# Kernel optimization log

Hardware: AMD Instinct MI355X
Metric: run time of the kernel (lower is better)

Reference implementation:

```python
import jax, jax.numpy as jnp
import numpy as np

B, T, ZDIM, H = 16384, 60, 6, 100
ATEMP = 5.0


def setup_inputs() -> dict:
    key = jax.random.key(0)
    ks = jax.random.split(key, 12)
    sampled_z = jax.random.normal(ks[0], (B, ZDIM), jnp.float32)
    u = jax.random.uniform(ks[1], (B, 5), jnp.float32)
    # physically plausible, strictly positive IDM params:
    # desired_v ~ [20,30], tgap ~ [1,2], min_jamx ~ [1,4], max/min act ~ [1,3]
    idm_params = jnp.stack([20. + 10. * u[:, 0], 1. + u[:, 1], 1. + 3. * u[:, 2],
                            1. + 2. * u[:, 3], 1. + 2. * u[:, 4]], axis=-1)
    # idm_s cols: [ego_v, f_v, m_v, ego_x, f_x, m_x, ef_dv, ef_dx, em_dv, em_dx, f_exists, m_exists]
    vels = jax.random.uniform(ks[2], (B, T, 3), jnp.float32, 0., 30.)
    glx = jax.random.uniform(ks[3], (B, T, 3), jnp.float32, 0., 500.)
    dvs = jax.random.normal(ks[4], (B, T, 2), jnp.float32) * 2.0
    dxs = jax.random.uniform(ks[5], (B, T, 2), jnp.float32, 5., 100.)
    ex = (jax.random.uniform(ks[6], (B, T, 2)) > 0.2).astype(jnp.float32)
    idm_s = jnp.concatenate([vels[:, :, 0:1], vels[:, :, 1:2], vels[:, :, 2:3],
                             glx[:, :, 0:1], glx[:, :, 1:2], glx[:, :, 2:3],
                             dvs[:, :, 0:1], dxs[:, :, 0:1],
                             dvs[:, :, 1:2], dxs[:, :, 1:2], ex], axis=-1)
    sdv_acts = jax.random.normal(ks[7], (B, T, 1), jnp.float32) * 0.5
    W1 = jax.random.normal(ks[8], (ZDIM, H), jnp.float32) * 0.1
    b1 = jnp.zeros((H,), jnp.float32)
    Wi = jax.random.normal(ks[9], (H + 1, 4 * H), jnp.float32) * 0.1
    Wh = jax.random.normal(ks[10], (H, 4 * H), jnp.float32) * 0.1
    bl = jnp.zeros((4 * H,), jnp.float32)
    Wa = jax.random.normal(ks[11], (H, 1), jnp.float32) * 0.1
    ba = jnp.zeros((1,), jnp.float32)
    return dict(sampled_z=sampled_z, idm_params=idm_params, idm_s=idm_s, sdv_acts=sdv_acts,
                W1=W1, b1=b1, Wi=Wi, Wh=Wh, bl=bl, Wa=Wa, ba=ba)


def _idm_driver(vel, dv, dx, p):
    dx = jnp.clip(dx, 0.5, 1000.0)
    desired_v, tgap, jamx = p[:, 0:1], p[:, 1:2], p[:, 2:3]
    amax, amin = p[:, 3:4], p[:, 4:5]
    gap = jamx + jax.nn.relu(tgap * vel + vel * dv / (2.0 * jnp.sqrt(amax * amin)))
    act = amax * (1.0 - (vel / desired_v) ** 4 - (gap / dx) ** 2)
    return jnp.clip(act, -3.0, 3.0)  # action_clip


def reference(sampled_z, idm_params, idm_s, sdv_acts, W1, b1, Wi, Wh, bl, Wa, ba):
    Bn = sampled_z.shape[0]
    proj = sampled_z @ W1 + b1                       # [B,100] latent projection
    nkey = jax.random.key(42)
    noise_f = jax.random.normal(jax.random.fold_in(nkey, 0), (T, Bn, 1), proj.dtype) * 0.5
    noise_m = jax.random.normal(jax.random.fold_in(nkey, 1), (T, Bn, 1), proj.dtype) * 0.5
    s_seq = jnp.transpose(idm_s, (1, 0, 2))          # [T,B,12]
    a_seq = jnp.transpose(sdv_acts, (1, 0, 2))       # [T,B,1]

    def step(carry, xs):
        ego_v, ego_x, prev_act, h, c = carry
        s, sdv, nf, nm, t = xs
        is0 = (t == 0)
        ego_v = jnp.where(is0, s[:, 0:1], ego_v + prev_act * 0.1)
        ego_x = jnp.where(is0, s[:, 3:4], ego_x + ego_v * 0.1 + 0.5 * prev_act * 0.01)
        fex, mex = s[:, 10:11], s[:, 11:12]
        ef_dx = (s[:, 4:5] - ego_x) * fex + (1.0 - fex) * s[:, 7:8]
        em_dx = (s[:, 5:6] - ego_x) * mex + (1.0 - mex) * s[:, 9:10]
        ef_dv = (ego_v - s[:, 1:2]) * fex + (1.0 - fex) * s[:, 6:7]
        em_dv = (ego_v - s[:, 2:3]) * mex + (1.0 - mex) * s[:, 8:9]
        ef_act = _idm_driver(ego_v, ef_dv, ef_dx, idm_params)
        ef_act = fex * ef_act + (1.0 - fex) * nf      # add_noise for nonexisting cars
        em_act = _idm_driver(ego_v, em_dv, em_dx, idm_params)
        em_act = mex * em_act + (1.0 - mex) * nm
        x = jnp.concatenate([proj, sdv], axis=-1)     # [B,101]
        z = x @ Wi + h @ Wh + bl                      # [B,400], keras gate order i,f,g,o
        i, f, g, o = jnp.split(z, 4, axis=-1)
        c = jax.nn.sigmoid(f) * c + jax.nn.sigmoid(i) * jnp.tanh(g)
        h = jax.nn.sigmoid(o) * jnp.tanh(c)
        att = jax.nn.sigmoid(ATEMP * (h @ Wa + ba))   # 1/(1+exp(-temp*x))
        act = (1.0 - att) * ef_act + att * em_act
        return (ego_v, ego_x, act, h, c), (act, att)

    z0 = jnp.zeros((Bn, 1), proj.dtype)
    carry0 = (z0, z0, z0, proj, proj)
    _, (acts, atts) = jax.lax.scan(step, carry0, (s_seq, a_seq, noise_f, noise_m, jnp.arange(T)))
    return jnp.transpose(acts, (1, 0, 2)), jnp.transpose(atts, (1, 0, 2))
```

## Files before the change

### kernel.cpp

```cpp
#include <hip/hip_runtime.h>
#include <cstdint>
#include <cstddef>

#define BTOT   16384
#define TSTEPS 60
#define HDIM   100
#define GDIM   400
#define NB     64
#define NTHR   1024

static_assert(BTOT % NB == 0, "batch tiling");

typedef __attribute__((ext_vector_type(8))) short bf16x8;
typedef __attribute__((ext_vector_type(4))) float f32x4;
typedef __attribute__((ext_vector_type(4))) unsigned int u32x4;

struct TFPair { uint32_t a, b; };

__host__ __device__ constexpr uint32_t rotl32c(uint32_t v, int r){
  return (v << r) | (v >> (32 - r));
}

__host__ __device__ constexpr TFPair tf2x32(uint32_t k0, uint32_t k1,
                                            uint32_t x0, uint32_t x1){
  const uint32_t ks2 = k0 ^ k1 ^ 0x1BD11BDAu;
  x0 += k0; x1 += k1;
  x0 += x1; x1 = rotl32c(x1,13); x1 ^= x0;
  x0 += x1; x1 = rotl32c(x1,15); x1 ^= x0;
  x0 += x1; x1 = rotl32c(x1,26); x1 ^= x0;
  x0 += x1; x1 = rotl32c(x1, 6); x1 ^= x0;
  x0 += k1;  x1 += ks2 + 1u;
  x0 += x1; x1 = rotl32c(x1,17); x1 ^= x0;
  x0 += x1; x1 = rotl32c(x1,29); x1 ^= x0;
  x0 += x1; x1 = rotl32c(x1,16); x1 ^= x0;
  x0 += x1; x1 = rotl32c(x1,24); x1 ^= x0;
  x0 += ks2; x1 += k0 + 2u;
  x0 += x1; x1 = rotl32c(x1,13); x1 ^= x0;
  x0 += x1; x1 = rotl32c(x1,15); x1 ^= x0;
  x0 += x1; x1 = rotl32c(x1,26); x1 ^= x0;
  x0 += x1; x1 = rotl32c(x1, 6); x1 ^= x0;
  x0 += k0;  x1 += k1 + 3u;
  x0 += x1; x1 = rotl32c(x1,17); x1 ^= x0;
  x0 += x1; x1 = rotl32c(x1,29); x1 ^= x0;
  x0 += x1; x1 = rotl32c(x1,16); x1 ^= x0;
  x0 += x1; x1 = rotl32c(x1,24); x1 ^= x0;
  x0 += k1;  x1 += ks2 + 4u;
  x0 += x1; x1 = rotl32c(x1,13); x1 ^= x0;
  x0 += x1; x1 = rotl32c(x1,15); x1 ^= x0;
  x0 += x1; x1 = rotl32c(x1,26); x1 ^= x0;
  x0 += x1; x1 = rotl32c(x1, 6); x1 ^= x0;
  x0 += ks2; x1 += k0 + 5u;
  return TFPair{x0, x1};
}

constexpr TFPair KF = tf2x32(0u, 42u, 0u, 0u);
constexpr TFPair KM = tf2x32(0u, 42u, 0u, 1u);

__device__ __forceinline__ float rcp_fast(float x){ return __builtin_amdgcn_rcpf(x); }
__device__ __forceinline__ float sigmoid_f(float x){ return rcp_fast(1.f + __expf(-x)); }
__device__ __forceinline__ float tanh_f(float x){
  float e = __expf(2.f * x);
  return 1.f - 2.f * rcp_fast(e + 1.f);
}

__device__ __forceinline__ float tf_noise(uint32_t k0, uint32_t k1, uint32_t n){
  TFPair r = tf2x32(k0, k1, 0u, n);
  uint32_t bits = r.a ^ r.b;
  float u = __uint_as_float((bits >> 9) | 0x3f800000u) - 1.0f;
  const float LOV = -0.99999994f;
  float v = fmaxf(LOV, fmaf(u, 2.0f, LOV));
  float w = -log1pf(-v * v);
  float p;
  if (w < 5.0f){
    w -= 2.5f;
    p =              2.81022636e-08f;
    p = fmaf(p, w,   3.43273939e-07f);
    p = fmaf(p, w,  -3.5233877e-06f);
    p = fmaf(p, w,  -4.39150654e-06f);
    p = fmaf(p, w,   0.00021858087f);
    p = fmaf(p, w,  -0.00125372503f);
    p = fmaf(p, w,  -0.00417768164f);
    p = fmaf(p, w,   0.246640727f);
    p = fmaf(p, w,   1.50140941f);
  } else {
    w = sqrtf(w) - 3.0f;
    p =             -0.000200214257f;
    p = fmaf(p, w,   0.000100950558f);
    p = fmaf(p, w,   0.00134934322f);
    p = fmaf(p, w,  -0.00367342844f);
    p = fmaf(p, w,   0.00573950773f);
    p = fmaf(p, w,  -0.0076224613f);
    p = fmaf(p, w,   0.00943887047f);
    p = fmaf(p, w,   1.00167406f);
    p = fmaf(p, w,   2.83297682f);
  }
  return 0.70710678f * (p * v);
}

__device__ __forceinline__ float idm_act(float vel, float dv, float dx,
                                         float v0, float tg, float jx,
                                         float am, float an){
  dx = fminf(fmaxf(dx, 0.5f), 1000.0f);
  float gap = jx + fmaxf(0.0f, tg*vel + vel*dv / (2.0f * sqrtf(am*an)));
  float r  = vel / v0;  float r2 = r*r;
  float gd = gap / dx;
  float a  = am * (1.0f - r2*r2 - gd*gd);
  return fminf(fmaxf(a, -3.0f), 3.0f);
}

__device__ __forceinline__ unsigned short f2bf(float f){
  uint32_t x = __float_as_uint(f);
  return (unsigned short)((x + 0x7fffu + ((x >> 16) & 1u)) >> 16);
}
__device__ __forceinline__ float bf2f(unsigned short h){
  return __uint_as_float(((uint32_t)h) << 16);
}

#define FRG_PACKETS (25*4*64)
#define WS_WI_HI 51200
#define WS_WI_LO 102400
#define WHF_HW   51200

__global__ void build_frags_kernel(const float* __restrict__ Wi,
                                   const float* __restrict__ Wh,
                                   unsigned short* __restrict__ ws){
  int p = blockIdx.x * 256 + threadIdx.x;
  if (p >= FRG_PACKETS) return;
  int lane = p & 63;
  int kf   = (p >> 6) & 3;
  int mt   = p >> 8;
  int zc   = mt*16 + (lane & 15);
  int orig = (zc & 3)*100 + (zc >> 2);
  int kb   = kf*32 + ((lane >> 4) << 3);
  #pragma unroll
  for (int j = 0; j < 8; ++j){
    int k = kb + j;
    float vh = (k < HDIM) ? Wh[(size_t)k*GDIM + orig] : 0.f;
    float vi = (k < HDIM) ? Wi[(size_t)k*GDIM + orig] : 0.f;
    unsigned short ih = f2bf(vi);
    ws[p*8 + j]            = f2bf(vh);
    ws[WS_WI_HI + p*8 + j] = ih;
    ws[WS_WI_LO + p*8 + j] = f2bf(vi - bf2f(ih));
  }
}

#define HBF_HW (2*4*4*512)
__device__ __forceinline__ int hfr_idx(int hl, int bt, int kf, int lp, int j){
  return (((hl*4 + bt)*4 + kf)*512 + lp*8 + j);
}

__device__ __forceinline__ void mfma1(f32x4 (&acc)[4][2],
                                      const unsigned short* __restrict__ whf,
                                      const unsigned short* __restrict__ hbf,
                                      int nmt, int mt0, int bt0, int lane){
  #pragma unroll
  for (int kf = 0; kf < 4; ++kf){
    bf16x8 Bh0 = *(const bf16x8*)&hbf[hfr_idx(0, bt0+0, kf, lane, 0)];
    bf16x8 Bh1 = *(const bf16x8*)&hbf[hfr_idx(0, bt0+1, kf, lane, 0)];
    #pragma unroll
    for (int m = 0; m < 4; ++m){
      if (m < nmt){
        bf16x8 Ah = *(const bf16x8*)&whf[((mt0 + m)*4 + kf)*512 + lane*8];
        acc[m][0] = __builtin_amdgcn_mfma_f32_16x16x32_bf16(Ah, Bh0, acc[m][0], 0,0,0);
        acc[m][1] = __builtin_amdgcn_mfma_f32_16x16x32_bf16(Ah, Bh1, acc[m][1], 0,0,0);
      }
    }
  }
}

__device__ __forceinline__ void mfma3_wi(f32x4 (&acc)[4][2],
                                         const unsigned short* __restrict__ frg,
                                         const unsigned short* __restrict__ hbf,
                                         int nmt, int mt0, int bt0, int lane){
  #pragma unroll
  for (int kf = 0; kf < 4; ++kf){
    bf16x8 Bh0 = *(const bf16x8*)&hbf[hfr_idx(0, bt0+0, kf, lane, 0)];
    bf16x8 Bl0 = *(const bf16x8*)&hbf[hfr_idx(1, bt0+0, kf, lane, 0)];
    bf16x8 Bh1 = *(const bf16x8*)&hbf[hfr_idx(0, bt0+1, kf, lane, 0)];
    bf16x8 Bl1 = *(const bf16x8*)&hbf[hfr_idx(1, bt0+1, kf, lane, 0)];
    #pragma unroll
    for (int m = 0; m < 4; ++m){
      if (m < nmt){
        int pidx = ((mt0 + m)*4 + kf)*64 + lane;
        bf16x8 Ah = *(const bf16x8*)(frg + WS_WI_HI + (size_t)pidx*8);
        bf16x8 Al = *(const bf16x8*)(frg + WS_WI_LO + (size_t)pidx*8);
        acc[m][0] = __builtin_amdgcn_mfma_f32_16x16x32_bf16(Ah, Bh0, acc[m][0], 0,0,0);
        acc[m][0] = __builtin_amdgcn_mfma_f32_16x16x32_bf16(Ah, Bl0, acc[m][0], 0,0,0);
        acc[m][0] = __builtin_amdgcn_mfma_f32_16x16x32_bf16(Al, Bh0, acc[m][0], 0,0,0);
        acc[m][1] = __builtin_amdgcn_mfma_f32_16x16x32_bf16(Ah, Bh1, acc[m][1], 0,0,0);
        acc[m][1] = __builtin_amdgcn_mfma_f32_16x16x32_bf16(Ah, Bl1, acc[m][1], 0,0,0);
        acc[m][1] = __builtin_amdgcn_mfma_f32_16x16x32_bf16(Al, Bh1, acc[m][1], 0,0,0);
      }
    }
  }
}

__global__ __attribute__((amdgpu_flat_work_group_size(NTHR, NTHR),
                          amdgpu_waves_per_eu(4, 4)))
void idm_sim_kernel(const float* __restrict__ sampled_z,
                    const float* __restrict__ idm_params,
                    const float* __restrict__ idm_s,
                    const float* __restrict__ sdv_acts,
                    const float* __restrict__ W1,
                    const float* __restrict__ b1,
                    const float* __restrict__ Wi,
                    const float* __restrict__ bl,
                    const float* __restrict__ Wa,
                    const float* __restrict__ ba,
                    const unsigned short* __restrict__ frg,
                    float* __restrict__ out)
{
  __shared__ __align__(16) unsigned short whf[WHF_HW];
  __shared__ __align__(16) unsigned short hbf[HBF_HW];
  __shared__ float part_lds[32*64];
  __shared__ float noise_lds[2][2][NB];
  __shared__ float blp_lds[GDIM];
  __shared__ float wi100p_lds[GDIM];

  const int tid  = threadIdx.x;
  const int lane = tid & 63;
  const int wid  = __builtin_amdgcn_readfirstlane(tid >> 6);
  const int b0   = blockIdx.x * NB;
  const int bg   = b0 + lane;

  const int bt0 = (wid >> 3) * 2;
  const int w8  = wid & 7;
  const int nmt = (w8 == 0) ? 1 : ((w8 == 7) ? 0 : 4);
  const int mt0 = (w8 == 0) ? 0 : 1 + (w8 - 1)*4;
  const int lg  = lane >> 4;
  const int li  = lane & 15;

  for (int i = tid; i < WHF_HW/8; i += NTHR)
    ((u32x4*)whf)[i] = ((const u32x4*)frg)[i];
  for (int i = tid; i < HBF_HW/8; i += NTHR)
    ((u32x4*)hbf)[i] = (u32x4)(0u);
  for (int i = tid; i < GDIM; i += NTHR){
    int g = i & 3, c = i >> 2;
    blp_lds[i]    = bl[g*100 + c];
    wi100p_lds[i] = Wi[(size_t)HDIM*GDIM + g*100 + c];
  }
  __syncthreads();

  for (int idx = tid; idx < HDIM*NB; idx += NTHR){
    int k = idx >> 6;
    int b = idx & 63;
    const float* szp = sampled_z + (size_t)(b0 + b) * 6;
    float v = b1[k];
    #pragma unroll
    for (int z = 0; z < 6; ++z) v = fmaf(szp[z], W1[z*HDIM + k], v);
    unsigned short hi = f2bf(v);
    unsigned short lo = f2bf(v - bf2f(hi));
    int bt = b >> 4;
    int kf = k >> 5, lp = (b & 15) + (((k & 31) >> 3) << 4), j = k & 7;
    hbf[hfr_idx(0, bt, kf, lp, j)] = hi;
    hbf[hfr_idx(1, bt, kf, lp, j)] = lo;
  }

  float wa_reg[4];
  float c_reg[4][2];
  #pragma unroll
  for (int m = 0; m < 4; ++m){
    if (m < nmt){
      int c = (mt0 + m)*4 + lg;
      wa_reg[m] = Wa[c];
      #pragma unroll
      for (int b2 = 0; b2 < 2; ++b2){
        int b = b0 + (bt0 + b2)*16 + li;
        const float* szp = sampled_z + (size_t)b * 6;
        float v = b1[c];
        #pragma unroll
        for (int z = 0; z < 6; ++z) v = fmaf(szp[z], W1[z*HDIM + c], v);
        c_reg[m][b2] = v;
      }
    }
  }
  __syncthreads();

  float xzs[4][2][4];
  if (nmt > 0){
    f32x4 acc[4][2];
    #pragma unroll
    for (int m = 0; m < 4; ++m){
      if (m < nmt){
        int zb = (mt0 + m)*16 + lg*4;
        f32x4 blv = *(const f32x4*)&blp_lds[zb];
        acc[m][0] = blv; acc[m][1] = blv;
      }
    }
    mfma3_wi(acc, frg, hbf, nmt, mt0, bt0, lane);
    #pragma unroll
    for (int m = 0; m < 4; ++m) if (m < nmt)
      #pragma unroll
      for (int b2 = 0; b2 < 2; ++b2)
        #pragma unroll
        for (int r = 0; r < 4; ++r) xzs[m][b2][r] = acc[m][b2][r];
  }

  float p_v0=0.f, p_tg=0.f, p_jx=0.f, p_am=0.f, p_an=0.f;
  if (wid == 0){
    const float* pp = idm_params + (size_t)bg * 5;
    p_v0 = pp[0]; p_tg = pp[1]; p_jx = pp[2]; p_am = pp[3]; p_an = pp[4];
  }
  float ego_v = 0.f, ego_x = 0.f, prev_act = 0.f;
  const float ba0 = ba[0];
  const int bb0 = b0 + bt0*16 + li;

  for (int t = 0; t < TSTEPS; ++t){
    float efa = 0.f, ema = 0.f, fex = 0.f, mex = 0.f;
    if (wid == 0){
      const float* sp = idm_s + ((size_t)bg * TSTEPS + t) * 12;
      float4 s0 = *(const float4*)(sp);
      float4 s1 = *(const float4*)(sp + 4);
      float4 s2 = *(const float4*)(sp + 8);
      if (t == 0){ ego_v = s0.x; ego_x = s0.w; }
      else {
        ego_v = ego_v + prev_act * 0.1f;
        ego_x = ego_x + ego_v * 0.1f + 0.5f * prev_act * 0.01f;
      }
      fex = s2.z; mex = s2.w;
      float ef_dx = (s1.x - ego_x)*fex + (1.f-fex)*s1.w;
      float em_dx = (s1.y - ego_x)*mex + (1.f-mex)*s2.y;
      float ef_dv = (ego_v - s0.y)*fex + (1.f-fex)*s1.z;
      float em_dv = (ego_v - s0.z)*mex + (1.f-mex)*s2.x;
      efa = idm_act(ego_v, ef_dv, ef_dx, p_v0, p_tg, p_jx, p_am, p_an);
      ema = idm_act(ego_v, em_dv, em_dx, p_v0, p_tg, p_jx, p_am, p_an);
    } else if (wid == 7){
      noise_lds[t & 1][0][lane] = tf_noise(KF.a, KF.b, (uint32_t)(t*BTOT + bg));
    } else if (wid == 15){
      noise_lds[t & 1][1][lane] = tf_noise(KM.a, KM.b, (uint32_t)(t*BTOT + bg));
    }

    f32x4 acc[4][2];
    if (nmt > 0){
      float sdv0 = sdv_acts[(size_t)bb0 * TSTEPS + t];
      float sdv1 = sdv_acts[(size_t)(bb0 + 16) * TSTEPS + t];
      #pragma unroll
      for (int m = 0; m < 4; ++m){
        if (m < nmt){
          int zb = (mt0 + m)*16 + lg*4;
          f32x4 wiv = *(const f32x4*)&wi100p_lds[zb];
          #pragma unroll
          for (int r = 0; r < 4; ++r){
            acc[m][0][r] = fmaf(sdv0, wiv[r], xzs[m][0][r]);
            acc[m][1][r] = fmaf(sdv1, wiv[r], xzs[m][1][r]);
          }
        }
      }
      mfma1(acc, whf, hbf, nmt, mt0, bt0, lane);
    }
    __syncthreads();

    float part0 = 0.f, part1 = 0.f;
    #pragma unroll
    for (int m = 0; m < 4; ++m){
      if (m < nmt){
        int c  = (mt0 + m)*4 + lg;
        int kf = c >> 5, lp = li + (((c & 31) >> 3) << 4), j = c & 7;
        #pragma unroll
        for (int b2 = 0; b2 < 2; ++b2){
          float zi = acc[m][b2][0];
          float zf = acc[m][b2][1];
          float zg = acc[m][b2][2];
          float zo = acc[m][b2][3];
          float cn = fmaf(sigmoid_f(zf), c_reg[m][b2], sigmoid_f(zi) * tanh_f(zg));
          c_reg[m][b2] = cn;
          float h = sigmoid_f(zo) * tanh_f(cn);
          hbf[hfr_idx(0, bt0 + b2, kf, lp, j)] = f2bf(h);
          float pw = h * wa_reg[m];
          if (b2 == 0) part0 += pw; else part1 += pw;
        }
      }
    }
    part_lds[(wid*2 + 0)*64 + lane] = part0;
    part_lds[(wid*2 + 1)*64 + lane] = part1;
    __syncthreads();

    if (wid == 0){
      int half = lane >> 5;
      int b2g  = (lane >> 4) & 1;
      int bi   = lane & 15;
      float dot = ba0;
      #pragma unroll
      for (int w = 0; w < 8; ++w)
        #pragma unroll
        for (int res = 0; res < 4; ++res)
          dot += part_lds[((half*8 + w)*2 + b2g)*64 + res*16 + bi];
      float att = sigmoid_f(5.0f * dot);
      float nf = noise_lds[t & 1][0][lane];
      float nm = noise_lds[t & 1][1][lane];
      float efb = fex*efa + (1.f-fex)*nf;
      float emb = mex*ema + (1.f-mex)*nm;
      float act = (1.f - att) * efb + att * emb;
      prev_act = act;
      out[(size_t)bg * TSTEPS + t] = act;
      out[(size_t)BTOT*TSTEPS + (size_t)bg * TSTEPS + t] = att;
    }
  }
}

extern "C" void kernel_launch(void* const* d_in, const int* in_sizes, int n_in,
                              void* d_out, int out_size, void* d_ws, size_t ws_size,
                              hipStream_t stream) {
  (void)in_sizes; (void)n_in; (void)ws_size; (void)out_size;
  const float* sampled_z  = (const float*)d_in[0];
  const float* idm_params = (const float*)d_in[1];
  const float* idm_s      = (const float*)d_in[2];
  const float* sdv_acts   = (const float*)d_in[3];
  const float* W1         = (const float*)d_in[4];
  const float* b1         = (const float*)d_in[5];
  const float* Wi         = (const float*)d_in[6];
  const float* Wh         = (const float*)d_in[7];
  const float* bl         = (const float*)d_in[8];
  const float* Wa         = (const float*)d_in[9];
  const float* ba         = (const float*)d_in[10];
  float* out = (float*)d_out;
  unsigned short* frg = (unsigned short*)d_ws;

  build_frags_kernel<<<25, 256, 0, stream>>>(Wi, Wh, frg);
  dim3 grid(BTOT / NB);
  dim3 block(NTHR);
  idm_sim_kernel<<<grid, block, 0, stream>>>(sampled_z, idm_params, idm_s, sdv_acts,
                                             W1, b1, Wi, bl, Wa, ba, frg, out);
}
```

Baseline: 338.2 us.

## Double-buffer LSTM hidden state and partials to drop one barrier per step

The hidden-state fragment buffer and the attention partial-sum buffer are double-buffered by step parity, which removes the barrier that used to sit between the MFMA read of h and the write of the new h. The idm_s and sdv_acts loads for the next step are issued one iteration early and carried in registers to hide global latency. The cost is extra LDS for a second copy of the h and partial buffers, plus extra live registers. Correctness depends on the single remaining barrier per step ordering the parity-indexed buffers correctly, and HBF_HW already reserves two halves.

After: 440.8 us. 1.3x slower.

```diff
diff --git a/kernel.cpp b/kernel.cpp
--- a/kernel.cpp
+++ b/kernel.cpp
@@ -152,11 +152,11 @@
 __device__ __forceinline__ void mfma1(f32x4 (&acc)[4][2],
                                       const unsigned short* __restrict__ whf,
                                       const unsigned short* __restrict__ hbf,
-                                      int nmt, int mt0, int bt0, int lane){
+                                      int cur, int nmt, int mt0, int bt0, int lane){
   #pragma unroll
   for (int kf = 0; kf < 4; ++kf){
-    bf16x8 Bh0 = *(const bf16x8*)&hbf[hfr_idx(0, bt0+0, kf, lane, 0)];
-    bf16x8 Bh1 = *(const bf16x8*)&hbf[hfr_idx(0, bt0+1, kf, lane, 0)];
+    bf16x8 Bh0 = *(const bf16x8*)&hbf[hfr_idx(cur, bt0+0, kf, lane, 0)];
+    bf16x8 Bh1 = *(const bf16x8*)&hbf[hfr_idx(cur, bt0+1, kf, lane, 0)];
     #pragma unroll
     for (int m = 0; m < 4; ++m){
       if (m < nmt){
@@ -212,7 +212,7 @@
 {
   __shared__ __align__(16) unsigned short whf[WHF_HW];
   __shared__ __align__(16) unsigned short hbf[HBF_HW];
-  __shared__ float part_lds[32*64];
+  __shared__ float part_lds[2][32*64];
   __shared__ float noise_lds[2][2][NB];
   __shared__ float blp_lds[GDIM];
   __shared__ float wi100p_lds[GDIM];
@@ -295,6 +295,7 @@
         #pragma unroll
         for (int r = 0; r < 4; ++r) xzs[m][b2][r] = acc[m][b2][r];
   }
+  __syncthreads();
 
   float p_v0=0.f, p_tg=0.f, p_jx=0.f, p_am=0.f, p_an=0.f;
   if (wid == 0){
@@ -305,35 +306,60 @@
   const float ba0 = ba[0];
   const int bb0 = b0 + bt0*16 + li;
 
+  float4 cs0 = {}, cs1 = {}, cs2 = {};
+  float csdv0 = 0.f, csdv1 = 0.f;
+  if (wid == 0){
+    const float* sp = idm_s + ((size_t)bg * TSTEPS + 0) * 12;
+    cs0 = *(const float4*)(sp);
+    cs1 = *(const float4*)(sp + 4);
+    cs2 = *(const float4*)(sp + 8);
+  }
+  if (nmt > 0){
+    csdv0 = sdv_acts[(size_t)bb0 * TSTEPS + 0];
+    csdv1 = sdv_acts[(size_t)(bb0 + 16) * TSTEPS + 0];
+  }
+
+  int cur = 0;
   for (int t = 0; t < TSTEPS; ++t){
+    const int nxt = cur ^ 1;
+    const int par = t & 1;
+    const int tp  = (t + 1 < TSTEPS) ? t + 1 : t;
+
+    float4 ns0, ns1, ns2;
+    float nsdv0, nsdv1;
+    if (wid == 0){
+      const float* sp = idm_s + ((size_t)bg * TSTEPS + tp) * 12;
+      ns0 = *(const float4*)(sp);
+      ns1 = *(const float4*)(sp + 4);
+      ns2 = *(const float4*)(sp + 8);
+    }
+    if (nmt > 0){
+      nsdv0 = sdv_acts[(size_t)bb0 * TSTEPS + tp];
+      nsdv1 = sdv_acts[(size_t)(bb0 + 16) * TSTEPS + tp];
+    }
+
     float efa = 0.f, ema = 0.f, fex = 0.f, mex = 0.f;
     if (wid == 0){
-      const float* sp = idm_s + ((size_t)bg * TSTEPS + t) * 12;
-      float4 s0 = *(const float4*)(sp);
-      float4 s1 = *(const float4*)(sp + 4);
-      float4 s2 = *(const float4*)(sp + 8);
-      if (t == 0){ ego_v = s0.x; ego_x = s0.w; }
+      if (t == 0){ ego_v = cs0.x; ego_x = cs0.w; }
       else {
         ego_v = ego_v + prev_act * 0.1f;
         ego_x = ego_x + ego_v * 0.1f + 0.5f * prev_act * 0.01f;
       }
-      fex = s2.z; mex = s2.w;
-      float ef_dx = (s1.x - ego_x)*fex + (1.f-fex)*s1.w;
-      float em_dx = (s1.y - ego_x)*mex + (1.f-mex)*s2.y;
-      float ef_dv = (ego_v - s0.y)*fex + (1.f-fex)*s1.z;
-      float em_dv = (ego_v - s0.z)*mex + (1.f-mex)*s2.x;
+      fex = cs2.z; mex = cs2.w;
+      float ef_dx = (cs1.x - ego_x)*fex + (1.f-fex)*cs1.w;
+      float em_dx = (cs1.y - ego_x)*mex + (1.f-mex)*cs2.y;
+      float ef_dv = (ego_v - cs0.y)*fex + (1.f-fex)*cs1.z;
+      float em_dv = (ego_v - cs0.z)*mex + (1.f-mex)*cs2.x;
       efa = idm_act(ego_v, ef_dv, ef_dx, p_v0, p_tg, p_jx, p_am, p_an);
       ema = idm_act(ego_v, em_dv, em_dx, p_v0, p_tg, p_jx, p_am, p_an);
     } else if (wid == 7){
-      noise_lds[t & 1][0][lane] = tf_noise(KF.a, KF.b, (uint32_t)(t*BTOT + bg));
+      noise_lds[par][0][lane] = tf_noise(KF.a, KF.b, (uint32_t)(t*BTOT + bg));
     } else if (wid == 15){
-      noise_lds[t & 1][1][lane] = tf_noise(KM.a, KM.b, (uint32_t)(t*BTOT + bg));
+      noise_lds[par][1][lane] = tf_noise(KM.a, KM.b, (uint32_t)(t*BTOT + bg));
     }
 
     f32x4 acc[4][2];
     if (nmt > 0){
-      float sdv0 = sdv_acts[(size_t)bb0 * TSTEPS + t];
-      float sdv1 = sdv_acts[(size_t)(bb0 + 16) * TSTEPS + t];
       #pragma unroll
       for (int m = 0; m < 4; ++m){
         if (m < nmt){
@@ -341,14 +367,13 @@
           f32x4 wiv = *(const f32x4*)&wi100p_lds[zb];
           #pragma unroll
           for (int r = 0; r < 4; ++r){
-            acc[m][0][r] = fmaf(sdv0, wiv[r], xzs[m][0][r]);
-            acc[m][1][r] = fmaf(sdv1, wiv[r], xzs[m][1][r]);
+            acc[m][0][r] = fmaf(csdv0, wiv[r], xzs[m][0][r]);
+            acc[m][1][r] = fmaf(csdv1, wiv[r], xzs[m][1][r]);
           }
         }
       }
-      mfma1(acc, whf, hbf, nmt, mt0, bt0, lane);
-    }
-    __syncthreads();
+      mfma1(acc, whf, hbf, cur, nmt, mt0, bt0, lane);
+    }
 
     float part0 = 0.f, part1 = 0.f;
     #pragma unroll
@@ -365,14 +390,14 @@
           float cn = fmaf(sigmoid_f(zf), c_reg[m][b2], sigmoid_f(zi) * tanh_f(zg));
           c_reg[m][b2] = cn;
           float h = sigmoid_f(zo) * tanh_f(cn);
-          hbf[hfr_idx(0, bt0 + b2, kf, lp, j)] = f2bf(h);
+          hbf[hfr_idx(nxt, bt0 + b2, kf, lp, j)] = f2bf(h);
           float pw = h * wa_reg[m];
           if (b2 == 0) part0 += pw; else part1 += pw;
         }
       }
     }
-    part_lds[(wid*2 + 0)*64 + lane] = part0;
-    part_lds[(wid*2 + 1)*64 + lane] = part1;
+    part_lds[par][(wid*2 + 0)*64 + lane] = part0;
+    part_lds[par][(wid*2 + 1)*64 + lane] = part1;
     __syncthreads();
 
     if (wid == 0){
@@ -384,10 +409,10 @@
       for (int w = 0; w < 8; ++w)
         #pragma unroll
         for (int res = 0; res < 4; ++res)
-          dot += part_lds[((half*8 + w)*2 + b2g)*64 + res*16 + bi];
+          dot += part_lds[par][((half*8 + w)*2 + b2g)*64 + res*16 + bi];
       float att = sigmoid_f(5.0f * dot);
-      float nf = noise_lds[t & 1][0][lane];
-      float nm = noise_lds[t & 1][1][lane];
+      float nf = noise_lds[par][0][lane];
+      float nm = noise_lds[par][1][lane];
       float efb = fex*efa + (1.f-fex)*nf;
       float emb = mex*ema + (1.f-mex)*nm;
       float act = (1.f - att) * efb + att * emb;
@@ -395,6 +420,10 @@
       out[(size_t)bg * TSTEPS + t] = act;
       out[(size_t)BTOT*TSTEPS + (size_t)bg * TSTEPS + t] = att;
     }
+
+    cs0 = ns0; cs1 = ns1; cs2 = ns2;
+    csdv0 = nsdv0; csdv1 = nsdv1;
+    cur = nxt;
   }
 }
 
```

## Double-buffer LSTM hidden state to drop one barrier per timestep

Applied to the files above, without the earlier changes.

The hidden-state bf16 fragments are ping-ponged between two LDS halves and the partial-dot buffer is doubled, so each timestep needs only one __syncthreads instead of two. The loop is unrolled by two with compile-time buffer indices, the sdv input projection is moved after the MFMA, and the tile ownership moves so wave 0 no longer does MFMA work alongside the IDM scalar path. The hi/lo half of hbf now serves as the second buffer, and correctness relies on the single barrier still ordering reads of the old buffer against writes to the new one.

Result: slower. 519.5 us (+53.6%).

```diff
diff --git a/kernel.cpp b/kernel.cpp
--- a/kernel.cpp
+++ b/kernel.cpp
@@ -10,6 +10,7 @@
 #define NTHR   1024
 
 static_assert(BTOT % NB == 0, "batch tiling");
+static_assert(TSTEPS % 2 == 0, "t-loop unrolled by 2");
 
 typedef __attribute__((ext_vector_type(8))) short bf16x8;
 typedef __attribute__((ext_vector_type(4))) float f32x4;
@@ -149,14 +150,15 @@
   return (((hl*4 + bt)*4 + kf)*512 + lp*8 + j);
 }
 
+template<int CUR>
 __device__ __forceinline__ void mfma1(f32x4 (&acc)[4][2],
                                       const unsigned short* __restrict__ whf,
                                       const unsigned short* __restrict__ hbf,
                                       int nmt, int mt0, int bt0, int lane){
   #pragma unroll
   for (int kf = 0; kf < 4; ++kf){
-    bf16x8 Bh0 = *(const bf16x8*)&hbf[hfr_idx(0, bt0+0, kf, lane, 0)];
-    bf16x8 Bh1 = *(const bf16x8*)&hbf[hfr_idx(0, bt0+1, kf, lane, 0)];
+    bf16x8 Bh0 = *(const bf16x8*)&hbf[hfr_idx(CUR, bt0+0, kf, lane, 0)];
+    bf16x8 Bh1 = *(const bf16x8*)&hbf[hfr_idx(CUR, bt0+1, kf, lane, 0)];
     #pragma unroll
     for (int m = 0; m < 4; ++m){
       if (m < nmt){
@@ -212,7 +214,7 @@
 {
   __shared__ __align__(16) unsigned short whf[WHF_HW];
   __shared__ __align__(16) unsigned short hbf[HBF_HW];
-  __shared__ float part_lds[32*64];
+  __shared__ float part_lds[2][32*64];
   __shared__ float noise_lds[2][2][NB];
   __shared__ float blp_lds[GDIM];
   __shared__ float wi100p_lds[GDIM];
@@ -225,20 +227,20 @@
 
   const int bt0 = (wid >> 3) * 2;
   const int w8  = wid & 7;
-  const int nmt = (w8 == 0) ? 1 : ((w8 == 7) ? 0 : 4);
-  const int mt0 = (w8 == 0) ? 0 : 1 + (w8 - 1)*4;
+  const int nmt = (w8 == 0) ? 0 : ((w8 == 7) ? 1 : 4);
+  const int mt0 = (w8 == 7) ? 24 : (w8 - 1)*4;
   const int lg  = lane >> 4;
   const int li  = lane & 15;
 
   for (int i = tid; i < WHF_HW/8; i += NTHR)
     ((u32x4*)whf)[i] = ((const u32x4*)frg)[i];
-  for (int i = tid; i < HBF_HW/8; i += NTHR)
-    ((u32x4*)hbf)[i] = (u32x4)(0u);
   for (int i = tid; i < GDIM; i += NTHR){
     int g = i & 3, c = i >> 2;
     blp_lds[i]    = bl[g*100 + c];
     wi100p_lds[i] = Wi[(size_t)HDIM*GDIM + g*100 + c];
   }
+  for (int i = tid; i < HBF_HW/8; i += NTHR)
+    ((u32x4*)hbf)[i] = (u32x4)(0u);
   __syncthreads();
 
   for (int idx = tid; idx < HDIM*NB; idx += NTHR){
@@ -295,6 +297,7 @@
         #pragma unroll
         for (int r = 0; r < 4; ++r) xzs[m][b2][r] = acc[m][b2][r];
   }
+  __syncthreads();
 
   float p_v0=0.f, p_tg=0.f, p_jx=0.f, p_am=0.f, p_an=0.f;
   if (wid == 0){
@@ -305,97 +308,110 @@
   const float ba0 = ba[0];
   const int bb0 = b0 + bt0*16 + li;
 
-  for (int t = 0; t < TSTEPS; ++t){
-    float efa = 0.f, ema = 0.f, fex = 0.f, mex = 0.f;
-    if (wid == 0){
-      const float* sp = idm_s + ((size_t)bg * TSTEPS + t) * 12;
-      float4 s0 = *(const float4*)(sp);
-      float4 s1 = *(const float4*)(sp + 4);
-      float4 s2 = *(const float4*)(sp + 8);
-      if (t == 0){ ego_v = s0.x; ego_x = s0.w; }
-      else {
-        ego_v = ego_v + prev_act * 0.1f;
-        ego_x = ego_x + ego_v * 0.1f + 0.5f * prev_act * 0.01f;
-      }
-      fex = s2.z; mex = s2.w;
-      float ef_dx = (s1.x - ego_x)*fex + (1.f-fex)*s1.w;
-      float em_dx = (s1.y - ego_x)*mex + (1.f-mex)*s2.y;
-      float ef_dv = (ego_v - s0.y)*fex + (1.f-fex)*s1.z;
-      float em_dv = (ego_v - s0.z)*mex + (1.f-mex)*s2.x;
-      efa = idm_act(ego_v, ef_dv, ef_dx, p_v0, p_tg, p_jx, p_am, p_an);
-      ema = idm_act(ego_v, em_dv, em_dx, p_v0, p_tg, p_jx, p_am, p_an);
-    } else if (wid == 7){
-      noise_lds[t & 1][0][lane] = tf_noise(KF.a, KF.b, (uint32_t)(t*BTOT + bg));
-    } else if (wid == 15){
-      noise_lds[t & 1][1][lane] = tf_noise(KM.a, KM.b, (uint32_t)(t*BTOT + bg));
-    }
-
-    f32x4 acc[4][2];
-    if (nmt > 0){
-      float sdv0 = sdv_acts[(size_t)bb0 * TSTEPS + t];
-      float sdv1 = sdv_acts[(size_t)(bb0 + 16) * TSTEPS + t];
-      #pragma unroll
-      for (int m = 0; m < 4; ++m){
-        if (m < nmt){
-          int zb = (mt0 + m)*16 + lg*4;
-          f32x4 wiv = *(const f32x4*)&wi100p_lds[zb];
-          #pragma unroll
-          for (int r = 0; r < 4; ++r){
-            acc[m][0][r] = fmaf(sdv0, wiv[r], xzs[m][0][r]);
-            acc[m][1][r] = fmaf(sdv1, wiv[r], xzs[m][1][r]);
-          }
-        }
-      }
-      mfma1(acc, whf, hbf, nmt, mt0, bt0, lane);
-    }
-    __syncthreads();
-
-    float part0 = 0.f, part1 = 0.f;
-    #pragma unroll
-    for (int m = 0; m < 4; ++m){
-      if (m < nmt){
-        int c  = (mt0 + m)*4 + lg;
-        int kf = c >> 5, lp = li + (((c & 31) >> 3) << 4), j = c & 7;
-        #pragma unroll
-        for (int b2 = 0; b2 < 2; ++b2){
-          float zi = acc[m][b2][0];
-          float zf = acc[m][b2][1];
-          float zg = acc[m][b2][2];
-          float zo = acc[m][b2][3];
-          float cn = fmaf(sigmoid_f(zf), c_reg[m][b2], sigmoid_f(zi) * tanh_f(zg));
-          c_reg[m][b2] = cn;
-          float h = sigmoid_f(zo) * tanh_f(cn);
-          hbf[hfr_idx(0, bt0 + b2, kf, lp, j)] = f2bf(h);
-          float pw = h * wa_reg[m];
-          if (b2 == 0) part0 += pw; else part1 += pw;
-        }
-      }
-    }
-    part_lds[(wid*2 + 0)*64 + lane] = part0;
-    part_lds[(wid*2 + 1)*64 + lane] = part1;
-    __syncthreads();
-
-    if (wid == 0){
-      int half = lane >> 5;
-      int b2g  = (lane >> 4) & 1;
-      int bi   = lane & 15;
-      float dot = ba0;
-      #pragma unroll
-      for (int w = 0; w < 8; ++w)
-        #pragma unroll
-        for (int res = 0; res < 4; ++res)
-          dot += part_lds[((half*8 + w)*2 + b2g)*64 + res*16 + bi];
-      float att = sigmoid_f(5.0f * dot);
-      float nf = noise_lds[t & 1][0][lane];
-      float nm = noise_lds[t & 1][1][lane];
-      float efb = fex*efa + (1.f-fex)*nf;
-      float emb = mex*ema + (1.f-mex)*nm;
-      float act = (1.f - att) * efb + att * emb;
-      prev_act = act;
-      out[(size_t)bg * TSTEPS + t] = act;
-      out[(size_t)BTOT*TSTEPS + (size_t)bg * TSTEPS + t] = att;
-    }
-  }
+#define STEP_BODY(T, CURB)                                                      \
+  {                                                                             \
+    const int t_ = (T);                                                         \
+     \
+    float sdv0 = 0.f, sdv1 = 0.f;                                               \
+    if (nmt > 0){                                                               \
+      sdv0 = sdv_acts[(size_t)bb0 * TSTEPS + t_];                               \
+      sdv1 = sdv_acts[(size_t)(bb0 + 16) * TSTEPS + t_];                        \
+    }                                                                           \
+    float efa = 0.f, ema = 0.f, fex = 0.f, mex = 0.f;                           \
+    if (wid == 0){                                                              \
+      const float* sp = idm_s + ((size_t)bg * TSTEPS + t_) * 12;                \
+      float4 s0 = *(const float4*)(sp);                                         \
+      float4 s1 = *(const float4*)(sp + 4);                                     \
+      float4 s2 = *(const float4*)(sp + 8);                                     \
+      if (t_ == 0){ ego_v = s0.x; ego_x = s0.w; }                               \
+      else {                                                                    \
+        ego_v = ego_v + prev_act * 0.1f;                                        \
+        ego_x = ego_x + ego_v * 0.1f + 0.5f * prev_act * 0.01f;                 \
+      }                                                                         \
+      fex = s2.z; mex = s2.w;                                                   \
+      float ef_dx = (s1.x - ego_x)*fex + (1.f-fex)*s1.w;                        \
+      float em_dx = (s1.y - ego_x)*mex + (1.f-mex)*s2.y;                        \
+      float ef_dv = (ego_v - s0.y)*fex + (1.f-fex)*s1.z;                        \
+      float em_dv = (ego_v - s0.z)*mex + (1.f-mex)*s2.x;                        \
+      efa = idm_act(ego_v, ef_dv, ef_dx, p_v0, p_tg, p_jx, p_am, p_an);         \
+      ema = idm_act(ego_v, em_dv, em_dx, p_v0, p_tg, p_jx, p_am, p_an);         \
+    } else if (wid == 7){                                                       \
+      noise_lds[CURB][0][lane] = tf_noise(KF.a, KF.b, (uint32_t)(t_*BTOT + bg));\
+    } else if (wid == 15){                                                      \
+      noise_lds[CURB][1][lane] = tf_noise(KM.a, KM.b, (uint32_t)(t_*BTOT + bg));\
+    }                                                                           \
+       \
+    f32x4 acc[4][2];                                                            \
+    if (nmt > 0){                                                               \
+      _Pragma("unroll")                                                         \
+      for (int m = 0; m < 4; ++m){                                              \
+        if (m < nmt){                                                           \
+          _Pragma("unroll")                                                     \
+          for (int r = 0; r < 4; ++r){                                          \
+            acc[m][0][r] = xzs[m][0][r];                                        \
+            acc[m][1][r] = xzs[m][1][r];                                        \
+          }                                                                     \
+        }                                                                       \
+      }                                                                         \
+      mfma1<CURB>(acc, whf, hbf, nmt, mt0, bt0, lane);                          \
+    }                                                                           \
+              \
+    float part0 = 0.f, part1 = 0.f;                                             \
+    _Pragma("unroll")                                                           \
+    for (int m = 0; m < 4; ++m){                                                \
+      if (m < nmt){                                                             \
+        int c  = (mt0 + m)*4 + lg;                                              \
+        int kf = c >> 5, lp = li + (((c & 31) >> 3) << 4), j = c & 7;           \
+        int zb = (mt0 + m)*16 + lg*4;                                           \
+        f32x4 wiv = *(const f32x4*)&wi100p_lds[zb];                             \
+        _Pragma("unroll")                                                       \
+        for (int b2 = 0; b2 < 2; ++b2){                                         \
+          float sdv = (b2 == 0) ? sdv0 : sdv1;                                  \
+          float zi = fmaf(sdv, wiv[0], acc[m][b2][0]);                          \
+          float zf = fmaf(sdv, wiv[1], acc[m][b2][1]);                          \
+          float zg = fmaf(sdv, wiv[2], acc[m][b2][2]);                          \
+          float zo = fmaf(sdv, wiv[3], acc[m][b2][3]);                          \
+          float cn = fmaf(sigmoid_f(zf), c_reg[m][b2],                          \
+                          sigmoid_f(zi) * tanh_f(zg));                          \
+          c_reg[m][b2] = cn;                                                    \
+          float h = sigmoid_f(zo) * tanh_f(cn);                                 \
+          hbf[hfr_idx((CURB)^1, bt0 + b2, kf, lp, j)] = f2bf(h);                \
+          float pw = h * wa_reg[m];                                             \
+          if (b2 == 0) part0 += pw; else part1 += pw;                           \
+        }                                                                       \
+      }                                                                         \
+    }                                                                           \
+    part_lds[CURB][(wid*2 + 0)*64 + lane] = part0;                              \
+    part_lds[CURB][(wid*2 + 1)*64 + lane] = part1;                              \
+    __syncthreads();     \
+         \
+    if (wid == 0){                                                              \
+      int half = lane >> 5;                                                     \
+      int b2g  = (lane >> 4) & 1;                                               \
+      int bi   = lane & 15;                                                     \
+      float dot = ba0;                                                          \
+      _Pragma("unroll")                                                         \
+      for (int w = 0; w < 8; ++w)                                               \
+        _Pragma("unroll")                                                       \
+        for (int res = 0; res < 4; ++res)                                       \
+          dot += part_lds[CURB][((half*8 + w)*2 + b2g)*64 + res*16 + bi];       \
+      float att = sigmoid_f(5.0f * dot);                                        \
+      float nf = noise_lds[CURB][0][lane];                                      \
+      float nm = noise_lds[CURB][1][lane];                                      \
+      float efb = fex*efa + (1.f-fex)*nf;                                       \
+      float emb = mex*ema + (1.f-mex)*nm;                                       \
+      float act = (1.f - att) * efb + att * emb;                                \
+      prev_act = act;                                                           \
+      out[(size_t)bg * TSTEPS + t_] = act;                                      \
+      out[(size_t)BTOT*TSTEPS + (size_t)bg * TSTEPS + t_] = att;                \
+    }                                                                           \
+  }
+
+  for (int t = 0; t < TSTEPS; t += 2){
+    STEP_BODY(t,     0)
+    STEP_BODY(t + 1, 1)
+  }
+#undef STEP_BODY
 }
 
 extern "C" void kernel_launch(void* const* d_in, const int* in_sizes, int n_in,
```
